# Optimization experiments

Hardware: AMD Instinct MI355X
Metric: run time of the kernel (lower is better)

Reference implementation:

```python
import jax, jax.numpy as jnp
import numpy as np

B, N, D = 2, 2048, 2048
H = 16
HD = D // H  # 128


def setup_inputs() -> dict:
    key = jax.random.key(0)
    k1, k2, k3 = jax.random.split(key, 3)
    x = jax.random.normal(k1, (B, N, D), dtype=jnp.float32)
    # Linear weights stored as [in, out] so y = x @ W matches torch's x @ W.T
    Wq = jax.random.normal(k2, (D, D), dtype=jnp.float32) * (D ** -0.5)
    Wo = jax.random.normal(k3, (D, D), dtype=jnp.float32) * (D ** -0.5)
    bo = jnp.zeros((D,), dtype=jnp.float32)
    return {"x": x, "Wq": Wq, "Wo": Wo, "bo": bo}


def reference(x, Wq, Wo, bo):
    # NOTE: source module (faithfully) projects q, k, v all with q_matrix.
    b, n, d = x.shape
    q = x @ Wq                                   # [B, N, D]
    qh = q.reshape(b, n, H, HD).transpose(0, 2, 1, 3)  # [B, H, N, HD]
    scores = jnp.einsum("bhnd,bhmd->bhnm", qh, qh) * (HD ** -0.5)  # [B,H,N,N]
    attn = jax.nn.softmax(scores, axis=-1)
    y = jnp.einsum("bhnm,bhmd->bhnd", attn, qh)  # [B, H, N, HD]
    y = y.transpose(0, 2, 1, 3).reshape(b, n, d)  # [B, N, D]
    return y @ Wo + bo
```

## Files before the change

### kernel.cpp

```cpp
#include <hip/hip_runtime.h>
#include <hip/hip_bf16.h>

#define BATCH 2
#define SEQ   2048
#define DIM   2048
#define NHEAD 16
#define HDIM  128

#define KSTRIDE 136
#define VSTRIDE 72
#define PSTRIDE 72

typedef __bf16 bf16;
typedef __attribute__((ext_vector_type(2))) __bf16 bf16x2;
typedef __attribute__((ext_vector_type(4))) __bf16 bf16x4;
typedef __attribute__((ext_vector_type(8))) __bf16 bf16x8;
typedef __attribute__((ext_vector_type(4))) float f32x4;

__device__ __forceinline__ void load_lds16(const bf16* g, bf16* l) {
    __builtin_amdgcn_global_load_lds((const __attribute__((address_space(1))) void*)g,
                                     (__attribute__((address_space(3))) void*)l, 16, 0, 0);
}

__device__ __forceinline__ float exp2_hw(float x) { return __builtin_amdgcn_exp2f(x); }

__global__ __launch_bounds__(256)
void prep_kernel(const float* __restrict__ x, bf16* __restrict__ xb,
                 const float* __restrict__ Wq, bf16* __restrict__ Wtq,
                 const float* __restrict__ Wo, bf16* __restrict__ Wto)
{
    __shared__ bf16 T[64 * 72];
    const int bid = blockIdx.x;
    if (bid < 4096) {
        const size_t i = ((size_t)bid * 256 + threadIdx.x) * 8;
        const float4 f0 = *(const float4*)(x + i);
        const float4 f1 = *(const float4*)(x + i + 4);
        *(bf16x8*)(xb + i) = (bf16x8){(bf16)f0.x, (bf16)f0.y, (bf16)f0.z, (bf16)f0.w,
                                      (bf16)f1.x, (bf16)f1.y, (bf16)f1.z, (bf16)f1.w};
        return;
    }
    int t = bid - 4096;
    const float* W  = (t < 1024) ? Wq : Wo;
    bf16*        Wt = (t < 1024) ? Wtq : Wto;
    t &= 1023;
    const int kb = (t >> 5) * 64, nb = (t & 31) * 64;

    const int a = threadIdx.x & 31;
    const int g = threadIdx.x >> 5;
    {
        const float* s0 = W + (size_t)(kb + 2 * a) * DIM + nb + g * 8;
        const float4 r0a = *(const float4*)(s0);
        const float4 r0b = *(const float4*)(s0 + 4);
        const float4 r1a = *(const float4*)(s0 + DIM);
        const float4 r1b = *(const float4*)(s0 + DIM + 4);
        float v0[8] = {r0a.x, r0a.y, r0a.z, r0a.w, r0b.x, r0b.y, r0b.z, r0b.w};
        float v1[8] = {r1a.x, r1a.y, r1a.z, r1a.w, r1b.x, r1b.y, r1b.z, r1b.w};
        #pragma unroll
        for (int i = 0; i < 8; ++i)
            *(bf16x2*)&T[(g * 8 + i) * 72 + 2 * a] = (bf16x2){(bf16)v0[i], (bf16)v1[i]};
    }
    __syncthreads();

    const int r  = threadIdx.x >> 2;
    const int k0 = (threadIdx.x & 3) * 16;
    bf16x8 o0 = *(const bf16x8*)&T[r * 72 + k0];
    bf16x8 o1 = *(const bf16x8*)&T[r * 72 + k0 + 8];
    *(bf16x8*)(Wt + (size_t)(nb + r) * DIM + kb + k0)     = o0;
    *(bf16x8*)(Wt + (size_t)(nb + r) * DIM + kb + k0 + 8) = o1;
}

template<bool OUT_F32_BIAS>
__global__ __launch_bounds__(256)
void gemm_bt(const bf16* __restrict__ A, const bf16* __restrict__ Bt,
             const float* __restrict__ bias, void* __restrict__ Cptr,
             int M, int N, int K)
{
    __shared__ bf16 As[2][128 * 32];
    __shared__ bf16 Bs[2][128 * 32];

    const int tid  = threadIdx.x;
    const int wave = tid >> 6;
    const int lane = tid & 63;
    const int quad = lane >> 4;
    const int l16  = lane & 15;
    const int wr   = (wave >> 1) * 64;
    const int wc   = (wave & 1) * 64;
    const int rowBase = blockIdx.y * 128;
    const int colBase = blockIdx.x * 128;

    const int srow = lane >> 2;
    const int scol = (lane & 3) * 8;
    const bf16* aBase = A  + (size_t)(rowBase + wave * 16 + srow) * K + scol;
    const bf16* bBase = Bt + (size_t)(colBase + wave * 16 + srow) * K + scol;

    f32x4 acc[4][4] = {};

    for (int k0 = 0; k0 < K; k0 += 64) {
        #pragma unroll
        for (int rh = 0; rh < 2; ++rh) {
            #pragma unroll
            for (int kh = 0; kh < 2; ++kh) {
                load_lds16(aBase + (size_t)rh * 64 * K + k0 + kh * 32,
                           (bf16*)As[kh] + (rh * 64 + wave * 16) * 32);
                load_lds16(bBase + (size_t)rh * 64 * K + k0 + kh * 32,
                           (bf16*)Bs[kh] + (rh * 64 + wave * 16) * 32);
            }
        }
        __syncthreads();

        #pragma unroll
        for (int ks = 0; ks < 2; ++ks) {
            bf16x8 a[4], b[4];
            #pragma unroll
            for (int i = 0; i < 4; ++i)
                a[i] = *(const bf16x8*)&As[ks][(wr + i * 16 + l16) * 32 + quad * 8];
            #pragma unroll
            for (int j = 0; j < 4; ++j)
                b[j] = *(const bf16x8*)&Bs[ks][(wc + j * 16 + l16) * 32 + quad * 8];
            #pragma unroll
            for (int i = 0; i < 4; ++i)
                #pragma unroll
                for (int j = 0; j < 4; ++j)
                    acc[i][j] = __builtin_amdgcn_mfma_f32_16x16x32_bf16(a[i], b[j], acc[i][j], 0, 0, 0);
        }
        __syncthreads();
    }

    #pragma unroll
    for (int i = 0; i < 4; ++i) {
        #pragma unroll
        for (int j = 0; j < 4; ++j) {
            #pragma unroll
            for (int r = 0; r < 4; ++r) {
                const int row = rowBase + wr + i * 16 + quad * 4 + r;
                const int col = colBase + wc + j * 16 + l16;
                const float v = acc[i][j][r];
                if (OUT_F32_BIAS) ((float*)Cptr)[(size_t)row * N + col] = v + bias[col];
                else              ((bf16*)Cptr)[(size_t)row * N + col] = (bf16)v;
            }
        }
    }
}

__global__ __launch_bounds__(256, 2)
void attn_kernel(const bf16* __restrict__ q, bf16* __restrict__ y)
{
    __shared__ bf16 Ks[64 * KSTRIDE];
    __shared__ bf16 Vt[HDIM * VSTRIDE];
    __shared__ bf16 Ps[128 * PSTRIDE];

    const int tid  = threadIdx.x;
    const int wave = tid >> 6;
    const int lane = tid & 63;
    const int quad = lane >> 4;
    const int l16  = lane & 15;

    const int p   = blockIdx.x;
    const int xcd = p & 7;
    const int pos = p >> 3;
    const int g   = xcd * 4 + (pos & 3);
    const int qt  = pos >> 2;
    const int h   = g & 15;
    const int bb  = g >> 4;

    const bf16* qb = q + (size_t)bb * SEQ * DIM + (size_t)h * HDIM;

    const float qs = 0.12752820031096662f;
    bf16x8 aq[2][4];
    #pragma unroll
    for (int nt = 0; nt < 2; ++nt) {
        #pragma unroll
        for (int ks = 0; ks < 4; ++ks) {
            const bf16* src = qb + (size_t)(qt * 128 + wave * 32 + nt * 16 + l16) * DIM + ks * 32 + quad * 8;
            bf16x8 v = *(const bf16x8*)src;
            bf16x8 o;
            #pragma unroll
            for (int e = 0; e < 8; ++e) o[e] = (bf16)((float)v[e] * qs);
            aq[nt][ks] = o;
        }
    }

    float lpart[2] = {0.f, 0.f};
    f32x4 yacc[2][8] = {};

    const int kr   = tid >> 2;
    const int koff = (tid & 3) * 32;
    const int sp   = tid & 31;
    const int ss   = tid >> 5;

    const bf16* srcK = qb + (size_t)kr * DIM + koff;
    const bf16* srcV = qb + (size_t)(2 * sp) * DIM + ss * 16;

    bf16x8 kreg[4], va[2], vb[2];
    #pragma unroll
    for (int c = 0; c < 4; ++c) kreg[c] = *(const bf16x8*)(srcK + c * 8);
    va[0] = *(const bf16x8*)(srcV + 0);
    va[1] = *(const bf16x8*)(srcV + 8);
    vb[0] = *(const bf16x8*)(srcV + DIM + 0);
    vb[1] = *(const bf16x8*)(srcV + DIM + 8);

    for (int kt = 0; kt < SEQ / 64; ++kt) {
        __syncthreads();

        #pragma unroll
        for (int c = 0; c < 4; ++c)
            *(bf16x8*)&Ks[kr * KSTRIDE + koff + c * 8] = kreg[c];
        #pragma unroll
        for (int c = 0; c < 2; ++c)
            #pragma unroll
            for (int e = 0; e < 8; ++e)
                *(bf16x2*)&Vt[(ss * 16 + c * 8 + e) * VSTRIDE + 2 * sp] = (bf16x2){va[c][e], vb[c][e]};

        if (kt + 1 < SEQ / 64) {
            const bf16* nK = srcK + (size_t)(kt + 1) * 64 * DIM;
            const bf16* nV = srcV + (size_t)(kt + 1) * 64 * DIM;
            #pragma unroll
            for (int c = 0; c < 4; ++c) kreg[c] = *(const bf16x8*)(nK + c * 8);
            va[0] = *(const bf16x8*)(nV + 0);
            va[1] = *(const bf16x8*)(nV + 8);
            vb[0] = *(const bf16x8*)(nV + DIM + 0);
            vb[1] = *(const bf16x8*)(nV + DIM + 8);
        }
        __syncthreads();

        #pragma unroll
        for (int mt = 0; mt < 4; ++mt) {
            bf16x8 ak[4];
            #pragma unroll
            for (int ks = 0; ks < 4; ++ks)
                ak[ks] = *(const bf16x8*)&Ks[(mt * 16 + l16) * KSTRIDE + ks * 32 + quad * 8];
            f32x4 s[2] = {};
            #pragma unroll
            for (int ks = 0; ks < 4; ++ks)
                #pragma unroll
                for (int nt = 0; nt < 2; ++nt)
                    s[nt] = __builtin_amdgcn_mfma_f32_16x16x32_bf16(ak[ks], aq[nt][ks], s[nt], 0, 0, 0);
            #pragma unroll
            for (int nt = 0; nt < 2; ++nt) {
                float p0 = exp2_hw(s[nt][0]);
                float p1 = exp2_hw(s[nt][1]);
                float p2 = exp2_hw(s[nt][2]);
                float p3 = exp2_hw(s[nt][3]);
                lpart[nt] += (p0 + p1) + (p2 + p3);
                *(bf16x4*)&Ps[(wave * 32 + nt * 16 + l16) * PSTRIDE + mt * 16 + quad * 4] =
                    (bf16x4){(bf16)p0, (bf16)p1, (bf16)p2, (bf16)p3};
            }
        }

        #pragma unroll
        for (int ks2 = 0; ks2 < 2; ++ks2) {
            bf16x8 ap[2];
            #pragma unroll
            for (int i = 0; i < 2; ++i)
                ap[i] = *(const bf16x8*)&Ps[(wave * 32 + i * 16 + l16) * PSTRIDE + ks2 * 32 + quad * 8];
            #pragma unroll
            for (int n = 0; n < 8; ++n) {
                bf16x8 bv = *(const bf16x8*)&Vt[(n * 16 + l16) * VSTRIDE + ks2 * 32 + quad * 8];
                #pragma unroll
                for (int i = 0; i < 2; ++i)
                    yacc[i][n] = __builtin_amdgcn_mfma_f32_16x16x32_bf16(ap[i], bv, yacc[i][n], 0, 0, 0);
            }
        }
    }

    float lfull[2];
    #pragma unroll
    for (int nt = 0; nt < 2; ++nt) {
        float l = lpart[nt];
        l += __shfl_xor(l, 16);
        l += __shfl_xor(l, 32);
        lfull[nt] = l;
    }

    bf16* yb = y + (size_t)bb * SEQ * DIM + (size_t)(qt * 128) * DIM + (size_t)h * HDIM;
    #pragma unroll
    for (int i = 0; i < 2; ++i) {
        #pragma unroll
        for (int r = 0; r < 4; ++r) {
            const float lv  = __shfl(lfull[i], (lane & 48) | (quad * 4 + r));
            const float inv = 1.f / lv;
            const int row = wave * 32 + i * 16 + quad * 4 + r;
            #pragma unroll
            for (int n = 0; n < 8; ++n)
                yb[(size_t)row * DIM + n * 16 + l16] = (bf16)(yacc[i][n][r] * inv);
        }
    }
}

extern "C" void kernel_launch(void* const* d_in, const int* in_sizes, int n_in,
                              void* d_out, int out_size, void* d_ws, size_t ws_size,
                              hipStream_t stream)
{
    const float* x  = (const float*)d_in[0];
    const float* Wq = (const float*)d_in[1];
    const float* Wo = (const float*)d_in[2];
    const float* bo = (const float*)d_in[3];
    float* out = (float*)d_out;

    const size_t NELEM = (size_t)BATCH * SEQ * DIM;
    bf16* qws = (bf16*)d_ws;
    bf16* yws = qws + NELEM;
    bf16* Wtq = yws;
    bf16* Wto = qws + 2 * NELEM;
    bf16* xb  = (bf16*)d_out;

    const int M = BATCH * SEQ;
    dim3 gg(DIM / 128, M / 128);

    prep_kernel<<<6144, 256, 0, stream>>>(x, xb, Wq, Wtq, Wo, Wto);
    gemm_bt<false><<<gg, 256, 0, stream>>>(xb, Wtq, nullptr, qws, M, DIM, DIM);
    attn_kernel<<<512, 256, 0, stream>>>(qws, yws);
    gemm_bt<true><<<gg, 256, 0, stream>>>(yws, Wto, bo, out, M, DIM, DIM);
}
```

Before: 279.8 us.

## Double-buffer GEMM LDS tiles with register-staged global prefetch

```diff
diff --git a/kernel.cpp b/kernel.cpp
--- a/kernel.cpp
+++ b/kernel.cpp
@@ -16,11 +16,6 @@
 typedef __attribute__((ext_vector_type(4))) __bf16 bf16x4;
 typedef __attribute__((ext_vector_type(8))) __bf16 bf16x8;
 typedef __attribute__((ext_vector_type(4))) float f32x4;
-
-__device__ __forceinline__ void load_lds16(const bf16* g, bf16* l) {
-    __builtin_amdgcn_global_load_lds((const __attribute__((address_space(1))) void*)g,
-                                     (__attribute__((address_space(3))) void*)l, 16, 0, 0);
-}
 
 __device__ __forceinline__ float exp2_hw(float x) { return __builtin_amdgcn_exp2f(x); }
 
@@ -75,8 +70,8 @@
              const float* __restrict__ bias, void* __restrict__ Cptr,
              int M, int N, int K)
 {
-    __shared__ bf16 As[2][128 * 32];
-    __shared__ bf16 Bs[2][128 * 32];
+    __shared__ bf16 As[2][2][128 * 32];
+    __shared__ bf16 Bs[2][2][128 * 32];
 
     const int tid  = threadIdx.x;
     const int wave = tid >> 6;
@@ -90,33 +85,67 @@
 
     const int srow = lane >> 2;
     const int scol = (lane & 3) * 8;
+    const int ldsOff = (wave * 16 + srow) * 32 + scol;
     const bf16* aBase = A  + (size_t)(rowBase + wave * 16 + srow) * K + scol;
     const bf16* bBase = Bt + (size_t)(colBase + wave * 16 + srow) * K + scol;
 
     f32x4 acc[4][4] = {};
+    bf16x8 pa[2][2], pb[2][2];
+
+    #pragma unroll
+    for (int rh = 0; rh < 2; ++rh)
+        #pragma unroll
+        for (int kh = 0; kh < 2; ++kh) {
+            pa[rh][kh] = *(const bf16x8*)(aBase + (size_t)rh * 64 * K + kh * 32);
+            pb[rh][kh] = *(const bf16x8*)(bBase + (size_t)rh * 64 * K + kh * 32);
+        }
+    #pragma unroll
+    for (int rh = 0; rh < 2; ++rh)
+        #pragma unroll
+        for (int kh = 0; kh < 2; ++kh) {
+            *(bf16x8*)&As[0][kh][rh * 2048 + ldsOff] = pa[rh][kh];
+            *(bf16x8*)&Bs[0][kh][rh * 2048 + ldsOff] = pb[rh][kh];
+        }
+    #pragma unroll
+    for (int rh = 0; rh < 2; ++rh)
+        #pragma unroll
+        for (int kh = 0; kh < 2; ++kh) {
+            pa[rh][kh] = *(const bf16x8*)(aBase + (size_t)rh * 64 * K + 64 + kh * 32);
+            pb[rh][kh] = *(const bf16x8*)(bBase + (size_t)rh * 64 * K + 64 + kh * 32);
+        }
+    __syncthreads();
 
     for (int k0 = 0; k0 < K; k0 += 64) {
-        #pragma unroll
-        for (int rh = 0; rh < 2; ++rh) {
-            #pragma unroll
-            for (int kh = 0; kh < 2; ++kh) {
-                load_lds16(aBase + (size_t)rh * 64 * K + k0 + kh * 32,
-                           (bf16*)As[kh] + (rh * 64 + wave * 16) * 32);
-                load_lds16(bBase + (size_t)rh * 64 * K + k0 + kh * 32,
-                           (bf16*)Bs[kh] + (rh * 64 + wave * 16) * 32);
-            }
-        }
-        __syncthreads();
+        const int buf = (k0 >> 6) & 1;
+
+        if (k0 + 64 < K) {
+            #pragma unroll
+            for (int rh = 0; rh < 2; ++rh)
+                #pragma unroll
+                for (int kh = 0; kh < 2; ++kh) {
+                    *(bf16x8*)&As[buf ^ 1][kh][rh * 2048 + ldsOff] = pa[rh][kh];
+                    *(bf16x8*)&Bs[buf ^ 1][kh][rh * 2048 + ldsOff] = pb[rh][kh];
+                }
+        }
+        if (k0 + 128 < K) {
+            #pragma unroll
+            for (int rh = 0; rh < 2; ++rh)
+                #pragma unroll
+                for (int kh = 0; kh < 2; ++kh) {
+                    pa[rh][kh] = *(const bf16x8*)(aBase + (size_t)rh * 64 * K + k0 + 128 + kh * 32);
+                    pb[rh][kh] = *(const bf16x8*)(bBase + (size_t)rh * 64 * K + k0 + 128 + kh * 32);
+                }
+        }
 
         #pragma unroll
         for (int ks = 0; ks < 2; ++ks) {
             bf16x8 a[4], b[4];
             #pragma unroll
             for (int i = 0; i < 4; ++i)
-                a[i] = *(const bf16x8*)&As[ks][(wr + i * 16 + l16) * 32 + quad * 8];
+                a[i] = *(const bf16x8*)&As[buf][ks][(wr + i * 16 + l16) * 32 + quad * 8];
             #pragma unroll
             for (int j = 0; j < 4; ++j)
-                b[j] = *(const bf16x8*)&Bs[ks][(wc + j * 16 + l16) * 32 + quad * 8];
+                b[j] = *(const bf16x8*)&Bs[buf][ks][(wc + j * 16 + l16) * 32 + quad * 8];
             #pragma unroll
             for (int i = 0; i < 4; ++i)
                 #pragma unroll
@@ -295,7 +324,6 @@
     const float* Wq = (const float*)d_in[1];
     const float* Wo = (const float*)d_in[2];
     const float* bo = (const float*)d_in[3];
-    float* out = (float*)d_out;
 
     const size_t NELEM = (size_t)BATCH * SEQ * DIM;
     bf16* qws = (bf16*)d_ws;
@@ -310,5 +338,5 @@
     prep_kernel<<<6144, 256, 0, stream>>>(x, xb, Wq, Wtq, Wo, Wto);
     gemm_bt<false><<<gg, 256, 0, stream>>>(xb, Wtq, nullptr, qws, M, DIM, DIM);
     attn_kernel<<<512, 256, 0, stream>>>(qws, yws);
-    gemm_bt<true><<<gg, 256, 0, stream>>>(yws, Wto, bo, out, M, DIM, DIM);
+    gemm_bt<true><<<gg, 256, 0, stream>>>(yws, Wto, bo, (float*)d_out, M, DIM, DIM);
 }
```

Result: no change. 281.4 us (+0.6%).
